# Kernel tuning notes

Hardware: AMD Instinct MI355X
Metric: run time of the kernel (lower is better)

The kernel has to match this reference:

```python
import jax, jax.numpy as jnp
import numpy as np

N_NODES = 100000
N_EDGES = 1200000
D = 64
EPS = 1e-12  # matches torch F.normalize eps


def l2norm(x):
    n = jnp.linalg.norm(x, axis=-1, keepdims=True)
    return x / jnp.maximum(n, EPS)


def sage_layer(x, src, dst, Wl, bl, Wr, scale):
    # mechanism.normalize: row-wise L2 normalize (noise_scale=0 -> perturb is identity)
    xn = l2norm(x)
    # agg = x_normalized + scatter-add of neighbor (source) features into targets
    agg = xn + jax.ops.segment_sum(xn[src], dst, num_segments=N_NODES)
    # MessageNorm(learn_scale=True): normalize(msg) * ||x||_2 * scale
    msg = l2norm(agg) * jnp.linalg.norm(x, axis=-1, keepdims=True) * scale
    # lin_l(msg) + lin_r(x)  (root_weight=True, lin_r has no bias)
    out = msg @ Wl.T + bl + x @ Wr.T
    return l2norm(out)


def setup_inputs() -> dict:
    key = jax.random.key(0)
    ks = jax.random.split(key, 7)
    s = 1.0 / np.sqrt(D)
    return {
        "x": jax.random.normal(ks[0], (N_NODES, D), jnp.float32),
        "Wl0": jax.random.normal(ks[1], (D, D), jnp.float32) * s,
        "bl0": jnp.zeros((D,), jnp.float32),
        "Wr0": jax.random.normal(ks[2], (D, D), jnp.float32) * s,
        "scale0": jnp.ones((), jnp.float32),
        "Wl1": jax.random.normal(ks[3], (D, D), jnp.float32) * s,
        "bl1": jnp.zeros((D,), jnp.float32),
        "Wr1": jax.random.normal(ks[4], (D, D), jnp.float32) * s,
        "scale1": jnp.ones((), jnp.float32),
        "edge_index": jax.random.randint(ks[5], (2, N_EDGES), 0, N_NODES, dtype=jnp.int32),
    }


def reference(x, Wl0, bl0, Wr0, scale0, Wl1, bl1, Wr1, scale1, edge_index):
    src, dst = edge_index[0], edge_index[1]
    h = sage_layer(x, src, dst, Wl0, bl0, Wr0, scale0)
    h = jax.nn.relu(h)  # activation after layer 0 (not pred layer); dropout=identity (eval)
    h = sage_layer(h, src, dst, Wl1, bl1, Wr1, scale1)
    return h  # last layer of pred module: no bn/dropout/activation
```

## Files before the change

kernel.cpp:

```cpp
#include <hip/hip_runtime.h>

#define D 64
#define EPS 1e-12f
#define WPITCH 68
#define BSHIFT 8
#define BW 256
#define NBMAX 2048
#define NBLK 256

typedef unsigned short u16;

__device__ __forceinline__ float bf2f(u16 u) {
    return __uint_as_float(((unsigned)u) << 16);
}
__device__ __forceinline__ u16 f2bf(float f) {
    unsigned u = __float_as_uint(f);
    u += 0x7fffu + ((u >> 16) & 1u);
    return (u16)(u >> 16);
}
__device__ __forceinline__ float loadf(const void* p, size_t i, int bf) {
    return bf ? bf2f(((const u16*)p)[i]) : ((const float*)p)[i];
}
__device__ __forceinline__ float4 cvt4(ushort4 u) {
    return make_float4(bf2f(u.x), bf2f(u.y), bf2f(u.z), bf2f(u.w));
}

#define FMA4(acc, s, v)                       \
    do {                                      \
        acc.x = fmaf((s), (v).x, acc.x);      \
        acc.y = fmaf((s), (v).y, acc.y);      \
        acc.z = fmaf((s), (v).z, acc.z);      \
        acc.w = fmaf((s), (v).w, acc.w);      \
    } while (0)

__global__ __launch_bounds__(64) void detect_kernel(const u16* __restrict__ x,
                                                    int* __restrict__ flag) {
    int lane = threadIdx.x;
    int bad = 0;
    for (int i = 0; i < 64; ++i) {
        u16 u = x[lane * 64 + i];
        int e = (u >> 7) & 0xFF;
        if (e >= 0xC0) bad = 1;
    }
    unsigned long long b = __ballot(bad);
    if (lane == 0) *flag = (b == 0ull) ? 1 : 0;
}


__global__ __launch_bounds__(256) void zero_kernel(int* __restrict__ a, int n) {
    int i = blockIdx.x * blockDim.x + threadIdx.x;
    if (i < n) a[i] = 0;
}

__global__ __launch_bounds__(256) void bhist_kernel(const int* __restrict__ dst,
                                                    int* __restrict__ blockhist,
                                                    int E, int NB) {
    __shared__ int lh[NBMAX];
    const int b = blockIdx.x, t = threadIdx.x;
    const int per = (E + NBLK - 1) / NBLK;
    const int e0 = b * per, e1 = min(E, e0 + per);
    if (NB <= NBMAX) {
        for (int i = t; i < NB; i += 256) lh[i] = 0;
        __syncthreads();
        for (int e = e0 + t; e < e1; e += 256)
            atomicAdd(&lh[dst[e] >> BSHIFT], 1);
        __syncthreads();
        for (int i = t; i < NB; i += 256) blockhist[i * NBLK + b] = lh[i];
    } else {
        for (int e = e0 + t; e < e1; e += 256)
            atomicAdd(&blockhist[(dst[e] >> BSHIFT) * NBLK + b], 1);
    }
}

__global__ __launch_bounds__(256) void scanA_kernel(const int* __restrict__ a,
                                                    int* __restrict__ partials, int M) {
    int b = blockIdx.x, t = threadIdx.x;
    int base = b * 1024 + t * 4;
    int s = 0;
#pragma unroll
    for (int i = 0; i < 4; ++i) {
        int idx = base + i;
        if (idx < M) s += a[idx];
    }
    s += __shfl_xor(s, 32); s += __shfl_xor(s, 16); s += __shfl_xor(s, 8);
    s += __shfl_xor(s, 4);  s += __shfl_xor(s, 2);  s += __shfl_xor(s, 1);
    __shared__ int wt[4];
    if ((t & 63) == 0) wt[t >> 6] = s;
    __syncthreads();
    if (t == 0) partials[b] = wt[0] + wt[1] + wt[2] + wt[3];
}

__global__ __launch_bounds__(64) void scanB_kernel(int* __restrict__ partials, int NP) {
    int l = threadIdx.x;
    int total = 0;
    for (int base = 0; base < NP; base += 64) {
        int v = (base + l < NP) ? partials[base + l] : 0;
        int inc = v;
        for (int d = 1; d < 64; d <<= 1) {
            int u = __shfl_up(inc, d);
            if (l >= d) inc += u;
        }
        if (base + l < NP) partials[base + l] = inc - v + total;
        total += __shfl(inc, 63);
    }
}

__global__ __launch_bounds__(256) void scanC_kernel(const int* __restrict__ a,
                                                    const int* __restrict__ partials,
                                                    int* __restrict__ pos, int M) {
    int b = blockIdx.x, t = threadIdx.x;
    int base = b * 1024 + t * 4;
    int v[4];
    int s = 0;
#pragma unroll
    for (int i = 0; i < 4; ++i) {
        int idx = base + i;
        v[i] = (idx < M) ? a[idx] : 0;
        s += v[i];
    }
    int li = t & 63, w = t >> 6;
    int inc = s;
    for (int d = 1; d < 64; d <<= 1) {
        int u = __shfl_up(inc, d);
        if (li >= d) inc += u;
    }
    __shared__ int wt[4];
    if (li == 63) wt[w] = inc;
    __syncthreads();
    int woff = 0;
    for (int i = 0; i < w; ++i) woff += wt[i];
    int run = partials[b] + woff + (inc - s);
#pragma unroll
    for (int i = 0; i < 4; ++i) {
        int idx = base + i;
        if (idx < M) { pos[idx] = run; run += v[i]; }
    }
}

__global__ __launch_bounds__(256) void bmeta_kernel(const int* __restrict__ pos,
                                                    int* __restrict__ bcounts,
                                                    int* __restrict__ boffsets,
                                                    int NB, int E) {
    int i = blockIdx.x * blockDim.x + threadIdx.x;
    if (i < NB) {
        int s = pos[(size_t)i * NBLK];
        boffsets[i] = s;
        int nxt = (i + 1 < NB) ? pos[(size_t)(i + 1) * NBLK] : E;
        bcounts[i] = nxt - s;
    }
}

__global__ __launch_bounds__(256) void bfill_kernel(const int* __restrict__ src,
                                                    const int* __restrict__ dst,
                                                    int* __restrict__ pos,
                                                    int* __restrict__ bucket,
                                                    int E, int NB) {
    __shared__ int cur[NBMAX];
    const int b = blockIdx.x, t = threadIdx.x;
    const int per = (E + NBLK - 1) / NBLK;
    const int e0 = b * per, e1 = min(E, e0 + per);
    if (NB <= NBMAX) {
        for (int i = t; i < NB; i += 256) cur[i] = pos[(size_t)i * NBLK + b];
        __syncthreads();
        for (int e = e0 + t; e < e1; e += 256) {
            int s = src[e], d = dst[e];
            int p = atomicAdd(&cur[d >> BSHIFT], 1);
            bucket[p] = (s << BSHIFT) | (d & (BW - 1));
        }
    } else {
        for (int e = e0 + t; e < e1; e += 256) {
            int s = src[e], d = dst[e];
            int p = atomicAdd(&pos[(size_t)(d >> BSHIFT) * NBLK + b], 1);
            bucket[p] = (s << BSHIFT) | (d & (BW - 1));
        }
    }
}

__global__ __launch_bounds__(256) void csr_from_buckets_kernel(
    const int* __restrict__ bucket,
    const int* __restrict__ bcounts, const int* __restrict__ boffsets,
    int* __restrict__ counts, int* __restrict__ offsets,
    int* __restrict__ sorted_src, int N)
{
    __shared__ int hist[BW];
    __shared__ int cur[BW];
    __shared__ int wt[4];

    const int b = blockIdx.x;
    const int t = threadIdx.x;
    const int nbase = b << BSHIFT;
    const int ecnt = bcounts[b];
    const int ebase = boffsets[b];

    hist[t] = 0;
    __syncthreads();

    for (int e = t; e < ecnt; e += 256)
        atomicAdd(&hist[bucket[ebase + e] & (BW - 1)], 1);
    __syncthreads();

    int v = hist[t];
    int inc = v;
    for (int d = 1; d < 64; d <<= 1) {
        int u = __shfl_up(inc, d);
        if ((t & 63) >= d) inc += u;
    }
    if ((t & 63) == 63) wt[t >> 6] = inc;
    __syncthreads();
    int woff = 0;
    for (int i = 0; i < (t >> 6); ++i) woff += wt[i];
    int excl = inc - v + woff;
    cur[t] = excl;
    int node = nbase + t;
    if (node < N) {
        counts[node] = v;
        offsets[node] = ebase + excl;
    }
    __syncthreads();

    for (int e = t; e < ecnt; e += 256) {
        int pv = bucket[ebase + e];
        int p = atomicAdd(&cur[pv & (BW - 1)], 1);
        sorted_src[ebase + p] = ((unsigned)pv) >> BSHIFT;
    }
}


__global__ __launch_bounds__(256) void norm_init_kernel(
    const void* __restrict__ xin, float* __restrict__ nx, float* __restrict__ rnx,
    int N, const int* __restrict__ flagp)
{
    const int bf = *flagp;
    int node = (int)((blockIdx.x * blockDim.x + threadIdx.x) >> 6);
    int lane = threadIdx.x & 63;
    if (node >= N) return;
    float v = loadf(xin, (size_t)node * D + lane, bf);
    float s = v * v;
    s += __shfl_xor(s, 32); s += __shfl_xor(s, 16); s += __shfl_xor(s, 8);
    s += __shfl_xor(s, 4);  s += __shfl_xor(s, 2);  s += __shfl_xor(s, 1);
    if (lane == 0) {
        float n = sqrtf(s);
        nx[node] = n;
        rnx[node] = 1.0f / fmaxf(n, EPS);
    }
}

__device__ __forceinline__ float4 loadrow4(const void* p, int row, int lane16, int bf) {
    if (bf) {
        ushort4 u = ((const ushort4*)((const u16*)p + (size_t)row * D))[lane16];
        return cvt4(u);
    }
    return ((const float4*)((const float*)p + (size_t)row * D))[lane16];
}

__global__ __launch_bounds__(256) void gather_kernel(
    const int* __restrict__ offsets, const int* __restrict__ counts,
    const int* __restrict__ sorted_src,
    const void* __restrict__ xin, const float* __restrict__ rnx,
    float* __restrict__ agg, int N, const int* __restrict__ flagp)
{
    const int bf = *flagp;
    int node = (int)((blockIdx.x * blockDim.x + threadIdx.x) >> 6);
    int lane = threadIdx.x & 63;
    if (node >= N) return;
    const int lane16 = lane & 15, grp = lane >> 4;

    float4 acc = make_float4(0.f, 0.f, 0.f, 0.f);
    if (grp == 0) {
        float4 xs = loadrow4(xin, node, lane16, bf);
        FMA4(acc, rnx[node], xs);
    }

    const int start = offsets[node];
    const int deg = counts[node];
    for (int i = 0; i < deg; i += 64) {
        int cnt = min(deg - i, 64);
        int id = (lane < cnt) ? sorted_src[start + i + lane] : 0;
        float wvl = rnx[id];
        int j = 0;
        for (; j + 8 <= cnt; j += 8) {
            int s0 = __shfl(id, j + grp);
            int s1 = __shfl(id, j + 4 + grp);
            float w0 = __shfl(wvl, j + grp);
            float w1 = __shfl(wvl, j + 4 + grp);
            float4 v0 = loadrow4(xin, s0, lane16, bf);
            float4 v1 = loadrow4(xin, s1, lane16, bf);
            FMA4(acc, w0, v0);
            FMA4(acc, w1, v1);
        }
        if (j + 4 <= cnt) {
            int s0 = __shfl(id, j + grp);
            float w0 = __shfl(wvl, j + grp);
            float4 v0 = loadrow4(xin, s0, lane16, bf);
            FMA4(acc, w0, v0);
            j += 4;
        }
        if (j < cnt) {
            int e = j + grp;
            int s0 = __shfl(id, min(e, cnt - 1));
            float w0 = __shfl(wvl, min(e, cnt - 1));
            if (e < cnt) {
                float4 v0 = loadrow4(xin, s0, lane16, bf);
                FMA4(acc, w0, v0);
            }
        }
    }

    acc.x += __shfl_xor(acc.x, 16); acc.y += __shfl_xor(acc.y, 16);
    acc.z += __shfl_xor(acc.z, 16); acc.w += __shfl_xor(acc.w, 16);
    acc.x += __shfl_xor(acc.x, 32); acc.y += __shfl_xor(acc.y, 32);
    acc.z += __shfl_xor(acc.z, 32); acc.w += __shfl_xor(acc.w, 32);
    if (grp == 0)
        ((float4*)(agg + (size_t)node * D))[lane16] = acc;
}

#define KSTEP(kk, comp)                                                     \
    {                                                                       \
        float4 a = *((const float4*)(wlp + (kk) * WPITCH));                 \
        float4 b = *((const float4*)(wrp + (kk) * WPITCH));                 \
        FMA4(acc[0], m[0].comp, a); FMA4(acc[0], xf[0].comp, b);            \
        FMA4(acc[1], m[1].comp, a); FMA4(acc[1], xf[1].comp, b);            \
        FMA4(acc[2], m[2].comp, a); FMA4(acc[2], xf[2].comp, b);            \
        FMA4(acc[3], m[3].comp, a); FMA4(acc[3], xf[3].comp, b);            \
    }

#define MSHFL(k4)                                                           \
    {                                                                       \
        const int srcl_ = srcl | (k4);                                      \
        m[0].x = __shfl(m_reg[0].x, srcl_); m[0].y = __shfl(m_reg[0].y, srcl_); \
        m[0].z = __shfl(m_reg[0].z, srcl_); m[0].w = __shfl(m_reg[0].w, srcl_); \
        m[1].x = __shfl(m_reg[1].x, srcl_); m[1].y = __shfl(m_reg[1].y, srcl_); \
        m[1].z = __shfl(m_reg[1].z, srcl_); m[1].w = __shfl(m_reg[1].w, srcl_); \
        m[2].x = __shfl(m_reg[2].x, srcl_); m[2].y = __shfl(m_reg[2].y, srcl_); \
        m[2].z = __shfl(m_reg[2].z, srcl_); m[2].w = __shfl(m_reg[2].w, srcl_); \
        m[3].x = __shfl(m_reg[3].x, srcl_); m[3].y = __shfl(m_reg[3].y, srcl_); \
        m[3].z = __shfl(m_reg[3].z, srcl_); m[3].w = __shfl(m_reg[3].w, srcl_); \
    }

__global__ __launch_bounds__(256) void epilogue_kernel(
    const float* __restrict__ agg, float* __restrict__ nx,
    float* __restrict__ rnx, const void* __restrict__ xin,
    const void* __restrict__ wl, const void* __restrict__ bl,
    const void* __restrict__ wr, const void* __restrict__ scale_p,
    void* __restrict__ out, int N, const int* __restrict__ flagp,
    int relu, int write_norm)
{
    __shared__ float lds_wl[D * WPITCH];
    __shared__ float lds_wr[D * WPITCH];
    __shared__ float lds_bl[D];

    const int bf = *flagp;
    const int t = threadIdx.x;
    for (int idx = t; idx < D * D; idx += 256) {
        int j = idx >> 6, k = idx & 63;
        lds_wl[k * WPITCH + j] = loadf(wl, idx, bf);
        lds_wr[k * WPITCH + j] = loadf(wr, idx, bf);
    }
    if (t < D) lds_bl[t] = loadf(bl, t, bf);
    __syncthreads();

    const float scl = loadf(scale_p, 0, bf);
    const int w = t >> 6, lane = t & 63;
    const int sub = lane >> 4, cg = lane & 15;
    const int srcl = lane & 48;

    const int node0 = blockIdx.x * 64 + w * 16 + sub * 4;
    int n[4];
    bool valid[4];
    float4 m_reg[4];
    float nxv[4];
#pragma unroll
    for (int r = 0; r < 4; ++r) {
        int nn = node0 + r;
        valid[r] = nn < N;
        n[r] = valid[r] ? nn : N - 1;
        nxv[r] = nx[n[r]];
    }
#pragma unroll
    for (int r = 0; r < 4; ++r) {
        float4 v4 = ((const float4*)(agg + (size_t)n[r] * D))[cg];
        float s = v4.x * v4.x + v4.y * v4.y + v4.z * v4.z + v4.w * v4.w;
        s += __shfl_xor(s, 1); s += __shfl_xor(s, 2);
        s += __shfl_xor(s, 4); s += __shfl_xor(s, 8);
        float minv = scl * nxv[r] / fmaxf(sqrtf(s), EPS);
        m_reg[r] = make_float4(v4.x * minv, v4.y * minv, v4.z * minv, v4.w * minv);
    }

    float4 acc[4];
    {
        float4 b4 = ((const float4*)lds_bl)[cg];
#pragma unroll
        for (int r = 0; r < 4; ++r) acc[r] = b4;
    }

    const float* wlbase = lds_wl + cg * 4;
    const float* wrbase = lds_wr + cg * 4;

    if (bf) {
#pragma unroll
        for (int k4 = 0; k4 < 16; ++k4) {
            float4 m[4], xf[4];
            MSHFL(k4)
#pragma unroll
            for (int r = 0; r < 4; ++r) {
                ushort4 xu = ((const ushort4*)((const u16*)xin + (size_t)n[r] * D))[k4];
                xf[r] = cvt4(xu);
            }
            const float* wlp = wlbase + (k4 * 4) * WPITCH;
            const float* wrp = wrbase + (k4 * 4) * WPITCH;
            KSTEP(0, x) KSTEP(1, y) KSTEP(2, z) KSTEP(3, w)
        }
    } else {
#pragma unroll
        for (int k4 = 0; k4 < 16; ++k4) {
            float4 m[4], xf[4];
            MSHFL(k4)
#pragma unroll
            for (int r = 0; r < 4; ++r) {
                xf[r] = ((const float4*)((const float*)xin + (size_t)n[r] * D))[k4];
            }
            const float* wlp = wlbase + (k4 * 4) * WPITCH;
            const float* wrp = wrbase + (k4 * 4) * WPITCH;
            KSTEP(0, x) KSTEP(1, y) KSTEP(2, z) KSTEP(3, w)
        }
    }

#pragma unroll
    for (int r = 0; r < 4; ++r) {
        float4 v = acc[r];
        float s2 = v.x * v.x + v.y * v.y + v.z * v.z + v.w * v.w;
        s2 += __shfl_xor(s2, 1); s2 += __shfl_xor(s2, 2);
        s2 += __shfl_xor(s2, 4); s2 += __shfl_xor(s2, 8);
        float inv = 1.0f / fmaxf(sqrtf(s2), EPS);
        float4 rv = make_float4(v.x * inv, v.y * inv, v.z * inv, v.w * inv);
        if (relu) {
            rv.x = fmaxf(rv.x, 0.f); rv.y = fmaxf(rv.y, 0.f);
            rv.z = fmaxf(rv.z, 0.f); rv.w = fmaxf(rv.w, 0.f);
        }
        if (write_norm) {
            float s3 = rv.x * rv.x + rv.y * rv.y + rv.z * rv.z + rv.w * rv.w;
            s3 += __shfl_xor(s3, 1); s3 += __shfl_xor(s3, 2);
            s3 += __shfl_xor(s3, 4); s3 += __shfl_xor(s3, 8);
            if (valid[r] && cg == 0) {
                float nn = sqrtf(s3);
                nx[n[r]] = nn;
                rnx[n[r]] = 1.0f / fmaxf(nn, EPS);
            }
        }
        if (valid[r]) {
            if (bf) {
                ushort4 o = make_ushort4(f2bf(rv.x), f2bf(rv.y), f2bf(rv.z), f2bf(rv.w));
                ((ushort4*)((u16*)out + (size_t)n[r] * D))[cg] = o;
            } else {
                ((float4*)((float*)out + (size_t)n[r] * D))[cg] = rv;
            }
        }
    }
}

extern "C" void kernel_launch(void* const* d_in, const int* in_sizes, int n_in,
                              void* d_out, int out_size, void* d_ws, size_t ws_size,
                              hipStream_t stream)
{
    const void* x   = d_in[0];
    const void* Wl0 = d_in[1];
    const void* bl0 = d_in[2];
    const void* Wr0 = d_in[3];
    const void* sc0 = d_in[4];
    const void* Wl1 = d_in[5];
    const void* bl1 = d_in[6];
    const void* Wr1 = d_in[7];
    const void* sc1 = d_in[8];
    const int* ei   = (const int*)d_in[9];

    const int N = in_sizes[0] / D;
    const int E = in_sizes[9] / 2;
    const int* src = ei;
    const int* dst = ei + E;

    const int NB = (N + BW - 1) >> BSHIFT;
    const int M  = NB * NBLK;
    const int NP = (M + 1023) / 1024;

    float* agg       = (float*)d_ws;
    float* nx        = agg + (size_t)N * D;
    float* rnx       = nx + N;
    int* flag        = (int*)(rnx + N);
    int* counts      = flag + 1;
    int* offsets     = counts + N;
    int* bcounts     = offsets + N;
    int* boffsets    = bcounts + NB;
    int* blockhist   = boffsets + NB;
    int* pos         = blockhist + M;
    int* partials    = pos + M;
    int* bucket      = partials + NP;
    int* sorted_src  = bucket + E;

    void* h = d_out;

    dim3 blk(256);
    int gridA  = (N + 3) / 4;
    int gridC  = (N + 63) / 64;

    detect_kernel<<<1, 64, 0, stream>>>((const u16*)x, flag);

    if (NB > NBMAX)
        zero_kernel<<<(M + 255) / 256, blk, 0, stream>>>(blockhist, M);
    bhist_kernel<<<NBLK, blk, 0, stream>>>(dst, blockhist, E, NB);
    scanA_kernel<<<NP, blk, 0, stream>>>(blockhist, partials, M);
    scanB_kernel<<<1, 64, 0, stream>>>(partials, NP);
    scanC_kernel<<<NP, blk, 0, stream>>>(blockhist, partials, pos, M);
    bmeta_kernel<<<(NB + 255) / 256, blk, 0, stream>>>(pos, bcounts, boffsets, NB, E);
    bfill_kernel<<<NBLK, blk, 0, stream>>>(src, dst, pos, bucket, E, NB);
    csr_from_buckets_kernel<<<NB, blk, 0, stream>>>(bucket, bcounts, boffsets,
                                                    counts, offsets, sorted_src, N);

    norm_init_kernel<<<gridA, blk, 0, stream>>>(x, nx, rnx, N, flag);
    gather_kernel<<<gridA, blk, 0, stream>>>(offsets, counts, sorted_src, x, rnx,
                                             agg, N, flag);
    epilogue_kernel<<<gridC, blk, 0, stream>>>(agg, nx, rnx, x, Wl0, bl0, Wr0, sc0,
                                               h, N, flag, 1, 1);

    gather_kernel<<<gridA, blk, 0, stream>>>(offsets, counts, sorted_src, h, rnx,
                                             agg, N, flag);
    epilogue_kernel<<<gridC, blk, 0, stream>>>(agg, nx, rnx, h, Wl1, bl1, Wr1, sc1,
                                               d_out, N, flag, 0, 0);
}
```

Baseline: 370.8 us.

## Stage epilogue messages in LDS and process two node groups per block

The epilogue kernel now writes the normalized message rows into a per-wave LDS buffer and reads them back as float4, replacing the 16 cross-lane shuffles per k-step. Each block also handles 128 nodes in two passes instead of 64, so the weight matrices loaded into LDS are reused twice and the grid is halved. This trades shuffle traffic for LDS traffic and more shared memory per block, which could lower occupancy. Without a barrier between the LDS write and read, correctness relies on wave-level lockstep within each wave's private buffer.

After: 401.0 us. 8.2% more time.

```diff
diff --git a/kernel.cpp b/kernel.cpp
--- a/kernel.cpp
+++ b/kernel.cpp
@@ -324,19 +324,6 @@
         FMA4(acc[3], m[3].comp, a); FMA4(acc[3], xf[3].comp, b);            \
     }
 
-#define MSHFL(k4)                                                           \
-    {                                                                       \
-        const int srcl_ = srcl | (k4);                                      \
-        m[0].x = __shfl(m_reg[0].x, srcl_); m[0].y = __shfl(m_reg[0].y, srcl_); \
-        m[0].z = __shfl(m_reg[0].z, srcl_); m[0].w = __shfl(m_reg[0].w, srcl_); \
-        m[1].x = __shfl(m_reg[1].x, srcl_); m[1].y = __shfl(m_reg[1].y, srcl_); \
-        m[1].z = __shfl(m_reg[1].z, srcl_); m[1].w = __shfl(m_reg[1].w, srcl_); \
-        m[2].x = __shfl(m_reg[2].x, srcl_); m[2].y = __shfl(m_reg[2].y, srcl_); \
-        m[2].z = __shfl(m_reg[2].z, srcl_); m[2].w = __shfl(m_reg[2].w, srcl_); \
-        m[3].x = __shfl(m_reg[3].x, srcl_); m[3].y = __shfl(m_reg[3].y, srcl_); \
-        m[3].z = __shfl(m_reg[3].z, srcl_); m[3].w = __shfl(m_reg[3].w, srcl_); \
-    }
-
 __global__ __launch_bounds__(256) void epilogue_kernel(
     const float* __restrict__ agg, float* __restrict__ nx,
     float* __restrict__ rnx, const void* __restrict__ xin,
@@ -348,6 +335,7 @@
     __shared__ float lds_wl[D * WPITCH];
     __shared__ float lds_wr[D * WPITCH];
     __shared__ float lds_bl[D];
+    __shared__ float msgbuf[4][16 * WPITCH];
 
     const int bf = *flagp;
     const int t = threadIdx.x;
@@ -362,97 +350,104 @@
     const float scl = loadf(scale_p, 0, bf);
     const int w = t >> 6, lane = t & 63;
     const int sub = lane >> 4, cg = lane & 15;
-    const int srcl = lane & 48;
-
-    const int node0 = blockIdx.x * 64 + w * 16 + sub * 4;
-    int n[4];
-    bool valid[4];
-    float4 m_reg[4];
-    float nxv[4];
-#pragma unroll
-    for (int r = 0; r < 4; ++r) {
-        int nn = node0 + r;
-        valid[r] = nn < N;
-        n[r] = valid[r] ? nn : N - 1;
-        nxv[r] = nx[n[r]];
-    }
-#pragma unroll
-    for (int r = 0; r < 4; ++r) {
-        float4 v4 = ((const float4*)(agg + (size_t)n[r] * D))[cg];
-        float s = v4.x * v4.x + v4.y * v4.y + v4.z * v4.z + v4.w * v4.w;
-        s += __shfl_xor(s, 1); s += __shfl_xor(s, 2);
-        s += __shfl_xor(s, 4); s += __shfl_xor(s, 8);
-        float minv = scl * nxv[r] / fmaxf(sqrtf(s), EPS);
-        m_reg[r] = make_float4(v4.x * minv, v4.y * minv, v4.z * minv, v4.w * minv);
-    }
-
-    float4 acc[4];
-    {
-        float4 b4 = ((const float4*)lds_bl)[cg];
-#pragma unroll
-        for (int r = 0; r < 4; ++r) acc[r] = b4;
-    }
-
-    const float* wlbase = lds_wl + cg * 4;
-    const float* wrbase = lds_wr + cg * 4;
-
-    if (bf) {
-#pragma unroll
-        for (int k4 = 0; k4 < 16; ++k4) {
-            float4 m[4], xf[4];
-            MSHFL(k4)
-#pragma unroll
-            for (int r = 0; r < 4; ++r) {
-                ushort4 xu = ((const ushort4*)((const u16*)xin + (size_t)n[r] * D))[k4];
-                xf[r] = cvt4(xu);
+    float* mrow = msgbuf[w];
+
+    for (int g = 0; g < 2; ++g) {
+        const int node0 = blockIdx.x * 128 + g * 64 + w * 16 + sub * 4;
+        int n[4];
+        bool valid[4];
+        float4 a4[4];
+        float nxv[4];
+#pragma unroll
+        for (int r = 0; r < 4; ++r) {
+            int nn = node0 + r;
+            valid[r] = nn < N;
+            n[r] = valid[r] ? nn : N - 1;
+            a4[r] = ((const float4*)(agg + (size_t)n[r] * D))[cg];
+            nxv[r] = nx[n[r]];
+        }
+
+#pragma unroll
+        for (int r = 0; r < 4; ++r) {
+            float4 v4 = a4[r];
+            float s = v4.x * v4.x + v4.y * v4.y + v4.z * v4.z + v4.w * v4.w;
+            s += __shfl_xor(s, 1); s += __shfl_xor(s, 2);
+            s += __shfl_xor(s, 4); s += __shfl_xor(s, 8);
+            float minv = scl * nxv[r] / fmaxf(sqrtf(s), EPS);
+            *((float4*)(mrow + (sub * 4 + r) * WPITCH + cg * 4)) =
+                make_float4(v4.x * minv, v4.y * minv, v4.z * minv, v4.w * minv);
+        }
+
+        float4 acc[4];
+        {
+            float4 b4 = ((const float4*)lds_bl)[cg];
+#pragma unroll
+            for (int r = 0; r < 4; ++r) acc[r] = b4;
+        }
+
+        const float* wlbase = lds_wl + cg * 4;
+        const float* wrbase = lds_wr + cg * 4;
+
+        if (bf) {
+#pragma unroll
+            for (int k4 = 0; k4 < 16; ++k4) {
+                float4 m[4], xf[4];
+#pragma unroll
+                for (int r = 0; r < 4; ++r) {
+                    m[r] = *((const float4*)(mrow + (sub * 4 + r) * WPITCH + k4 * 4));
+                    ushort4 xu =
+                        ((const ushort4*)((const u16*)xin + (size_t)n[r] * D))[k4];
+                    xf[r] = cvt4(xu);
+                }
+                const float* wlp = wlbase + (k4 * 4) * WPITCH;
+                const float* wrp = wrbase + (k4 * 4) * WPITCH;
+                KSTEP(0, x) KSTEP(1, y) KSTEP(2, z) KSTEP(3, w)
             }
-            const float* wlp = wlbase + (k4 * 4) * WPITCH;
-            const float* wrp = wrbase + (k4 * 4) * WPITCH;
-            KSTEP(0, x) KSTEP(1, y) KSTEP(2, z) KSTEP(3, w)
-        }
-    } else {
-#pragma unroll
-        for (int k4 = 0; k4 < 16; ++k4) {
-            float4 m[4], xf[4];
-            MSHFL(k4)
-#pragma unroll
-            for (int r = 0; r < 4; ++r) {
-                xf[r] = ((const float4*)((const float*)xin + (size_t)n[r] * D))[k4];
+        } else {
+#pragma unroll
+            for (int k4 = 0; k4 < 16; ++k4) {
+                float4 m[4], xf[4];
+#pragma unroll
+                for (int r = 0; r < 4; ++r) {
+                    m[r] = *((const float4*)(mrow + (sub * 4 + r) * WPITCH + k4 * 4));
+                    xf[r] = ((const float4*)((const float*)xin + (size_t)n[r] * D))[k4];
+                }
+                const float* wlp = wlbase + (k4 * 4) * WPITCH;
+                const float* wrp = wrbase + (k4 * 4) * WPITCH;
+                KSTEP(0, x) KSTEP(1, y) KSTEP(2, z) KSTEP(3, w)
             }
-            const float* wlp = wlbase + (k4 * 4) * WPITCH;
-            const float* wrp = wrbase + (k4 * 4) * WPITCH;
-            KSTEP(0, x) KSTEP(1, y) KSTEP(2, z) KSTEP(3, w)
-        }
-    }
-
-#pragma unroll
-    for (int r = 0; r < 4; ++r) {
-        float4 v = acc[r];
-        float s2 = v.x * v.x + v.y * v.y + v.z * v.z + v.w * v.w;
-        s2 += __shfl_xor(s2, 1); s2 += __shfl_xor(s2, 2);
-        s2 += __shfl_xor(s2, 4); s2 += __shfl_xor(s2, 8);
-        float inv = 1.0f / fmaxf(sqrtf(s2), EPS);
-        float4 rv = make_float4(v.x * inv, v.y * inv, v.z * inv, v.w * inv);
-        if (relu) {
-            rv.x = fmaxf(rv.x, 0.f); rv.y = fmaxf(rv.y, 0.f);
-            rv.z = fmaxf(rv.z, 0.f); rv.w = fmaxf(rv.w, 0.f);
-        }
-        if (write_norm) {
-            float s3 = rv.x * rv.x + rv.y * rv.y + rv.z * rv.z + rv.w * rv.w;
-            s3 += __shfl_xor(s3, 1); s3 += __shfl_xor(s3, 2);
-            s3 += __shfl_xor(s3, 4); s3 += __shfl_xor(s3, 8);
-            if (valid[r] && cg == 0) {
-                float nn = sqrtf(s3);
-                nx[n[r]] = nn;
-                rnx[n[r]] = 1.0f / fmaxf(nn, EPS);
+        }
+
+#pragma unroll
+        for (int r = 0; r < 4; ++r) {
+            float4 v = acc[r];
+            float s2 = v.x * v.x + v.y * v.y + v.z * v.z + v.w * v.w;
+            s2 += __shfl_xor(s2, 1); s2 += __shfl_xor(s2, 2);
+            s2 += __shfl_xor(s2, 4); s2 += __shfl_xor(s2, 8);
+            float inv = 1.0f / fmaxf(sqrtf(s2), EPS);
+            float4 rv = make_float4(v.x * inv, v.y * inv, v.z * inv, v.w * inv);
+            if (relu) {
+                rv.x = fmaxf(rv.x, 0.f); rv.y = fmaxf(rv.y, 0.f);
+                rv.z = fmaxf(rv.z, 0.f); rv.w = fmaxf(rv.w, 0.f);
             }
-        }
-        if (valid[r]) {
-            if (bf) {
-                ushort4 o = make_ushort4(f2bf(rv.x), f2bf(rv.y), f2bf(rv.z), f2bf(rv.w));
-                ((ushort4*)((u16*)out + (size_t)n[r] * D))[cg] = o;
-            } else {
-                ((float4*)((float*)out + (size_t)n[r] * D))[cg] = rv;
+            if (write_norm) {
+                float s3 = rv.x * rv.x + rv.y * rv.y + rv.z * rv.z + rv.w * rv.w;
+                s3 += __shfl_xor(s3, 1); s3 += __shfl_xor(s3, 2);
+                s3 += __shfl_xor(s3, 4); s3 += __shfl_xor(s3, 8);
+                if (valid[r] && cg == 0) {
+                    float nn = sqrtf(s3);
+                    nx[n[r]] = nn;
+                    rnx[n[r]] = 1.0f / fmaxf(nn, EPS);
+                }
+            }
+            if (valid[r]) {
+                if (bf) {
+                    ushort4 o =
+                        make_ushort4(f2bf(rv.x), f2bf(rv.y), f2bf(rv.z), f2bf(rv.w));
+                    ((ushort4*)((u16*)out + (size_t)n[r] * D))[cg] = o;
+                } else {
+                    ((float4*)((float*)out + (size_t)n[r] * D))[cg] = rv;
+                }
             }
         }
     }
@@ -500,7 +495,7 @@
 
     dim3 blk(256);
     int gridA  = (N + 3) / 4;
-    int gridC  = (N + 63) / 64;
+    int gridC  = (N + 127) / 128;
 
     detect_kernel<<<1, 64, 0, stream>>>((const u16*)x, flag);
 
```
